# Kernel optimization log

Hardware: AMD Instinct MI355X
Metric: run time of the kernel (lower is better)

The kernel has to match this reference:

```python
import jax, jax.numpy as jnp
import numpy as np

B, N, C = 2, 2048, 2048
H, KV = 16, 4          # query heads, kv heads
D = C // H             # head_dim = 128
ROPE_BASE = 10000.0


def rope_cos_sin(position_ids, dim):
    # interleaved RoPE: freqs for even indices, repeated pairwise to full dim
    inv_freq = 1.0 / (ROPE_BASE ** (jnp.arange(0, dim, 2, dtype=jnp.float32) / dim))
    ang = position_ids[..., None].astype(jnp.float32) * inv_freq   # [B, N, D/2]
    cos = jnp.repeat(jnp.cos(ang), 2, axis=-1)                     # [B, N, D]
    sin = jnp.repeat(jnp.sin(ang), 2, axis=-1)
    return cos, sin


def rotate_half_interleaved(x):
    # (x0, x1, x2, x3, ...) -> (-x1, x0, -x3, x2, ...)
    x1 = x[..., 0::2]
    x2 = x[..., 1::2]
    return jnp.stack([-x2, x1], axis=-1).reshape(x.shape)


def apply_rotary(x, cos, sin):
    # x: [B, h, N, D]; cos/sin: [B, N, D]
    return x * cos[:, None] + rotate_half_interleaved(x) * sin[:, None]


def setup_inputs() -> dict:
    key = jax.random.key(0)
    ks = jax.random.split(key, 5)
    s = 0.02
    return dict(
        x=jax.random.normal(ks[0], (B, N, C), jnp.float32),
        position_ids=jnp.tile(jnp.arange(N, dtype=jnp.int32), (B, 1)),
        Wq=jax.random.normal(ks[1], (C, C), jnp.float32) * s,
        bq=jnp.zeros((C,), jnp.float32),
        Wk=jax.random.normal(ks[2], (C, KV * D), jnp.float32) * s,
        bk=jnp.zeros((KV * D,), jnp.float32),
        Wv=jax.random.normal(ks[3], (C, KV * D), jnp.float32) * s,
        bv=jnp.zeros((KV * D,), jnp.float32),
        Wo=jax.random.normal(ks[4], (C, C), jnp.float32) * s,
    )


def reference(x, position_ids, Wq, bq, Wk, bk, Wv, bv, Wo):
    Bx, Nx, Cx = x.shape
    q = (x @ Wq + bq).reshape(Bx, Nx, H, D).transpose(0, 2, 1, 3)   # [B,H,N,D]
    k = (x @ Wk + bk).reshape(Bx, Nx, KV, D).transpose(0, 2, 1, 3)  # [B,KV,N,D]
    v = (x @ Wv + bv).reshape(Bx, Nx, KV, D).transpose(0, 2, 1, 3)

    cos, sin = rope_cos_sin(position_ids, D)
    q = apply_rotary(q, cos, sin)
    k = apply_rotary(k, cos, sin)

    # GQA expand: head h uses kv head h // groups (matches unsqueeze+expand+reshape)
    groups = H // KV
    k = jnp.repeat(k, groups, axis=1)   # [B,H,N,D]
    v = jnp.repeat(v, groups, axis=1)

    attn = jnp.einsum('bhqd,bhkd->bhqk', q, k) * (D ** -0.5)        # [B,H,N,N]
    causal_mask = jnp.triu(jnp.ones((Nx, Nx), dtype=bool), 1)
    attn = jnp.where(causal_mask, -jnp.inf, attn)
    attn = jax.nn.softmax(attn, axis=-1)

    out = jnp.einsum('bhqk,bhkd->bhqd', attn, v)
    out = out.transpose(0, 2, 1, 3).reshape(Bx, Nx, Cx)
    return out @ Wo
```

## Files before the change

kernel.cpp:

```cpp
#include <hip/hip_runtime.h>
#include <cstdint>
#include <type_traits>

typedef unsigned short u16;
typedef unsigned int u32;
typedef __bf16 bf16x8 __attribute__((ext_vector_type(8)));
typedef float f32x4 __attribute__((ext_vector_type(4)));

constexpr int BB = 2;
constexpr int SEQ = 2048;
constexpr int CH = 2048;
constexpr int NH = 16;
constexpr int NKV = 4;
constexpr int HD = 128;
constexpr int QKVC = CH + 2 * NKV * HD;

#define DI __device__ __forceinline__

DI u16 f2b(float x) {
  u32 u = __float_as_uint(x);
  u = u + 0x7FFFu + ((u >> 16) & 1u);
  return (u16)(u >> 16);
}
DI float b2f(u16 u) { return __uint_as_float(((u32)u) << 16); }

DI u32 pack2bf(float lo, float hi) {
  return __builtin_amdgcn_perm(__float_as_uint(hi), __float_as_uint(lo), 0x07060302u);
}

DI void glds16(const void* g, void* l) {
  __builtin_amdgcn_global_load_lds(
      (__attribute__((address_space(1))) void*)(uintptr_t)g,
      (__attribute__((address_space(3))) void*)(u32)(uintptr_t)l, 16, 0, 0);
}

__global__ __launch_bounds__(256) void prep_kernel(
    const float* __restrict__ x, u16* __restrict__ xb,
    const float* __restrict__ Wq, const float* __restrict__ Wk,
    const float* __restrict__ Wv, const float* __restrict__ Wo,
    u16* __restrict__ wqkvt, u16* __restrict__ wot) {
  if (blockIdx.z == 4) {
    const int n4 = BB * SEQ * CH / 4;
    int base = (blockIdx.x + 32 * blockIdx.y) * 256 + threadIdx.x;
#pragma unroll
    for (int k = 0; k < 8; k++) {
      int i = base + k * 262144;
      if (i < n4) {
        float4 v = *(const float4*)&x[(size_t)i * 4];
        ushort4 o;
        o.x = f2b(v.x); o.y = f2b(v.y); o.z = f2b(v.z); o.w = f2b(v.w);
        *(ushort4*)&xb[(size_t)i * 4] = o;
      }
    }
    return;
  }
  const int z = blockIdx.z;
  const float* in;
  u16* out;
  int Cc;
  if (z == 0)      { in = Wq; out = wqkvt;                                Cc = CH; }
  else if (z == 1) { in = Wk; out = wqkvt + (size_t)CH * CH;              Cc = NKV * HD; }
  else if (z == 2) { in = Wv; out = wqkvt + (size_t)(CH + NKV * HD) * CH; Cc = NKV * HD; }
  else             { in = Wo; out = wot;                                  Cc = CH; }
  if ((int)blockIdx.y * 64 >= Cc) return;

  __shared__ u16 tile[64 * 65];
  const int r0 = blockIdx.x * 64, c0 = blockIdx.y * 64;
  const int tid = threadIdx.x;
  for (int c = tid; c < 1024; c += 256) {
    int r = c >> 4, col = (c & 15) * 4;
    float4 v = *(const float4*)&in[(size_t)(r0 + r) * Cc + c0 + col];
    tile[r * 65 + col + 0] = f2b(v.x);
    tile[r * 65 + col + 1] = f2b(v.y);
    tile[r * 65 + col + 2] = f2b(v.z);
    tile[r * 65 + col + 3] = f2b(v.w);
  }
  __syncthreads();
  for (int c = tid; c < 1024; c += 256) {
    int r = c >> 4, col = (c & 15) * 4;
    ushort4 v;
    v.x = tile[(col + 0) * 65 + r];
    v.y = tile[(col + 1) * 65 + r];
    v.z = tile[(col + 2) * 65 + r];
    v.w = tile[(col + 3) * 65 + r];
    *(ushort4*)&out[(size_t)(c0 + r) * CH + r0 + col] = v;
  }
}

__global__ __launch_bounds__(256) void vtrans_kernel(const u16* __restrict__ in,
                                                     u16* __restrict__ out) {
  __shared__ u16 tile[64 * 65];
  const int s = blockIdx.z, n0 = blockIdx.x * 64, d0 = blockIdx.y * 64;
  const int tid = threadIdx.x;
  const u16* ip = in + (size_t)s * SEQ * HD + (size_t)n0 * HD + d0;
  u16* op = out + (size_t)s * HD * SEQ + (size_t)d0 * SEQ + n0;
  for (int c = tid; c < 1024; c += 256) {
    int r = c >> 4, col = (c & 15) * 4;
    ushort4 v = *(const ushort4*)&ip[(size_t)r * HD + col];
    tile[r * 65 + col + 0] = v.x;
    tile[r * 65 + col + 1] = v.y;
    tile[r * 65 + col + 2] = v.z;
    tile[r * 65 + col + 3] = v.w;
  }
  __syncthreads();
  for (int c = tid; c < 1024; c += 256) {
    int r = c >> 4, col = (c & 15) * 4;
    ushort4 v;
    v.x = tile[(col + 0) * 65 + r];
    v.y = tile[(col + 1) * 65 + r];
    v.z = tile[(col + 2) * 65 + r];
    v.w = tile[(col + 3) * 65 + r];
    int u = col;
    int w = (u & 3) | (((u >> 5) & 1) << 2) | (((u >> 2) & 3) << 3) | (((u >> 4) & 1) << 5);
    int glp = (w >> 3) ^ (r & 7);
    int colp = glp * 8 + (w & 7);
    *(ushort4*)&op[(size_t)r * SEQ + colp] = v;
  }
}

template <int MODE>
__global__ __launch_bounds__(512, 2) void gemm256_kernel(
    const u16* __restrict__ A, const u16* __restrict__ Bt,
    u16* __restrict__ Qo, u16* __restrict__ Ko,
    float* __restrict__ Cf, u16* __restrict__ Vn,
    const float* __restrict__ bq, const float* __restrict__ bk,
    const float* __restrict__ bv, const int* __restrict__ pos,
    int M, int Nn, int K) {
  constexpr int BM = 128;
  constexpr int BN = (MODE == 0) ? 384 : 256;
  constexpr int NJ = (MODE == 0) ? 6 : 4;
  extern __shared__ char smem[];
  u16* As = (u16*)smem;
  u16* Bs = As + 2 * BM * 64;

  const int tid = threadIdx.x;
  const int lane = tid & 63, wave = tid >> 6;
  const int wrow = wave >> 2, wcol = wave & 3;
  const int lm = lane & 15, lq = lane >> 4;
  const int m0 = blockIdx.x * BM, n0 = blockIdx.y * BN;
  const int rr = tid >> 3;
  const int sswz8 = ((tid & 7) ^ (rr & 7)) * 8;

  f32x4 acc[4][NJ] = {};

  const int NT = K >> 6;

  if constexpr (MODE == 0) {
    auto stA = [&](int kt, int bsel, int h) {
      glds16(A + (size_t)(m0 + h * 64 + rr) * K + kt + sswz8,
             (char*)As + bsel * (BM * 128) + (h * 64 + wave * 8) * 128);
    };
    auto stB = [&](int kt, int bsel, int q, int s) {
      int g = 96 * ((s * 64 + rr) >> 5) + 32 * q + (rr & 31);
      glds16(Bt + (size_t)(n0 + g) * K + kt + sswz8,
             (char*)Bs + bsel * (BN * 128) + (q * 128 + s * 64 + wave * 8) * 128);
    };

    stA(0, 0, 0); stA(0, 0, 1);
    stB(0, 0, 0, 0); stB(0, 0, 0, 1);
    stB(0, 0, 1, 0); stB(0, 0, 1, 1);
    stB(0, 0, 2, 0); stB(0, 0, 2, 1);
    asm volatile("s_waitcnt vmcnt(0)" ::: "memory");
    __builtin_amdgcn_s_barrier();

    bf16x8 af[4][2];
    for (int T = 0; T < NT; T++) {
      const int buf = T & 1, nb = buf ^ 1;
      const u16* Asb = As + buf * (BM * 64);
      const u16* Bsb = Bs + buf * (BN * 64);
      const int kt1 = (T + 1) << 6;
      const bool pf = (T + 1 < NT);
#pragma unroll
      for (int q = 0; q < 3; q++) {
        if (q == 0) {
#pragma unroll
          for (int ii = 0; ii < 4; ii++)
#pragma unroll
            for (int kk = 0; kk < 2; kk++)
              af[ii][kk] = *(const bf16x8*)&Asb[(wrow * 64 + ii * 16 + lm) * 64 +
                                                ((kk * 4 + lq) ^ (lm & 7)) * 8];
        }
        bf16x8 bfq[2][2];
#pragma unroll
        for (int jj = 0; jj < 2; jj++)
#pragma unroll
          for (int kk = 0; kk < 2; kk++)
            bfq[jj][kk] = *(const bf16x8*)&Bsb[(q * 128 + wcol * 32 + jj * 16 + lm) * 64 +
                                               ((kk * 4 + lq) ^ (lm & 7)) * 8];
        if (pf) {
          if (q == 0) { stA(kt1, nb, 0); stA(kt1, nb, 1); stB(kt1, nb, 0, 0); stB(kt1, nb, 0, 1); }
          else if (q == 1) { stB(kt1, nb, 1, 0); stB(kt1, nb, 1, 1); }
          else { stB(kt1, nb, 2, 0); stB(kt1, nb, 2, 1); }
        }
        __builtin_amdgcn_s_barrier();
        asm volatile("s_waitcnt lgkmcnt(0)" ::: "memory");
        __builtin_amdgcn_sched_barrier(0);
        __builtin_amdgcn_s_setprio(1);
#pragma unroll
        for (int kk = 0; kk < 2; kk++)
#pragma unroll
          for (int ii = 0; ii < 4; ii++)
#pragma unroll
            for (int jj = 0; jj < 2; jj++)
              acc[ii][q * 2 + jj] = __builtin_amdgcn_mfma_f32_16x16x32_bf16(
                  af[ii][kk], bfq[jj][kk], acc[ii][q * 2 + jj], 0, 0, 0);
        __builtin_amdgcn_s_setprio(0);
        if (q == 0) {
          if (pf) asm volatile("s_waitcnt vmcnt(6)" ::: "memory");
          else    asm volatile("s_waitcnt vmcnt(2)" ::: "memory");
        } else if (q == 1) {
          if (pf) asm volatile("s_waitcnt vmcnt(6)" ::: "memory");
          else    asm volatile("s_waitcnt vmcnt(0)" ::: "memory");
        } else if (pf) {
          asm volatile("s_waitcnt vmcnt(4)" ::: "memory");
        }
        __builtin_amdgcn_s_barrier();
      }
    }
  } else {
    auto stageA = [&](int kt, int bsel, int half) {
      const int rb = (wave & 3) * 8 + (wave >> 2) * 64 + half * 32;
      glds16(A + (size_t)(m0 + rb + (lane >> 3)) * K + kt + sswz8,
             (char*)As + bsel * (BM * 128) + rb * 128);
    };
    auto stageB = [&](int kt, int bsel, int half) {
#pragma unroll
      for (int j = 0; j < 2; j++) {
        const int rb = (wave & 3) * 8 + (j * 2 + (wave >> 2)) * 64 + half * 32;
        glds16(Bt + (size_t)(n0 + rb + (lane >> 3)) * K + kt + sswz8,
               (char*)Bs + bsel * 32768 + rb * 128);
      }
    };

    stageA(0, 0, 0); stageB(0, 0, 0); stageB(0, 0, 1); stageA(0, 0, 1);
    asm volatile("s_waitcnt vmcnt(0)" ::: "memory");
    __builtin_amdgcn_s_barrier();

    bf16x8 bf1[4][2];
    for (int T = 0; T < NT; T++) {
      const int buf = T & 1;
      const u16* Asb = As + buf * (BM * 64);
      const u16* Bsb = Bs + buf * (256 * 64);
      const int kt1 = (T + 1) << 6;
      const bool pf = (T + 1 < NT);
      bf16x8 af[2][2];
#pragma unroll
      for (int q = 0; q < 2; q++) {
#pragma unroll
        for (int ii = 0; ii < 2; ii++)
#pragma unroll
          for (int kk = 0; kk < 2; kk++)
            af[ii][kk] = *(const bf16x8*)&Asb[(wrow * 64 + (q * 2 + ii) * 16 + lm) * 64 +
                                              ((kk * 4 + lq) ^ (lm & 7)) * 8];
        if (q == 0) {
#pragma unroll
          for (int j = 0; j < 4; j++)
#pragma unroll
            for (int kk = 0; kk < 2; kk++)
              bf1[j][kk] = *(const bf16x8*)&Bsb[(wcol * 64 + j * 16 + lm) * 64 +
                                                ((kk * 4 + lq) ^ (lm & 7)) * 8];
        }
        if (pf) {
          if (q == 0) { stageA(kt1, buf ^ 1, 0); stageB(kt1, buf ^ 1, 0); stageB(kt1, buf ^ 1, 1); }
          else stageA(kt1, buf ^ 1, 1);
        }
        __builtin_amdgcn_s_barrier();
        asm volatile("s_waitcnt lgkmcnt(0)" ::: "memory");
        __builtin_amdgcn_sched_barrier(0);
        __builtin_amdgcn_s_setprio(1);
#pragma unroll
        for (int kk = 0; kk < 2; kk++)
#pragma unroll
          for (int ii = 0; ii < 2; ii++)
#pragma unroll
            for (int j = 0; j < 4; j++)
              acc[q * 2 + ii][j] = __builtin_amdgcn_mfma_f32_16x16x32_bf16(
                  af[ii][kk], bf1[j][kk], acc[q * 2 + ii][j], 0, 0, 0);
        __builtin_amdgcn_s_setprio(0);
        if (q == 0) {
          if (pf) asm volatile("s_waitcnt vmcnt(5)" ::: "memory");
          else    asm volatile("s_waitcnt vmcnt(0)" ::: "memory");
        } else if (pf) {
          asm volatile("s_waitcnt vmcnt(1)" ::: "memory");
        }
        __builtin_amdgcn_s_barrier();
      }
    }
  }

  if constexpr (MODE == 0) {
    __syncthreads();
    float2* tab = (float2*)smem;
    const float LN1E4_64 = 0.14391156831212788f;
    for (int e = tid; e < 128 * 64; e += 512) {
      int tk = e >> 6, ii = e & 63;
      float ang = (float)pos[m0 + tk] * expf(-(float)ii * LN1E4_64);
      float sn, cs;
      sincosf(ang, &sn, &cs);
      tab[e] = make_float2(cs, sn);
    }
    __syncthreads();
    const float SCL2G = 0.12754325f;

#pragma unroll
    for (int i = 0; i < 4; i++) {
      const int mg = m0 + wrow * 64 + i * 16 + lq * 4;
#pragma unroll
      for (int j = 0; j < NJ; j++) {
        const int ng = n0 + wcol * 96 + j * 16 + lm;
        const int reg7 = (n0 + wcol * 96 + j * 16) >> 7;
        float bias = (ng < CH) ? bq[ng]
                               : (ng < CH + NKV * HD ? bk[ng - CH] : bv[ng - CH - NKV * HD]);
        if (reg7 < 16) {
          const int d = ng & 127, ii = d >> 1, hh = ng >> 7;
#pragma unroll
          for (int r = 0; r < 4; r++) {
            float v = acc[i][j][r] + bias;
            float vp = __shfl_xor(v, 1);
            float2 cw = tab[(mg + r - m0) * 64 + ii];
            float c = cw.x * SCL2G, s = cw.y * SCL2G;
            float o = fmaf(v, c, (lane & 1) ? vp * s : -(vp * s));
            int tok = mg + r, bb2 = tok >> 11, n = tok & (SEQ - 1);
            Qo[((size_t)(bb2 * NH + hh) * SEQ + n) * HD + d] = f2b(o);
          }
        } else if (reg7 < 20) {
          const int d = ng & 127, ii = d >> 1, kh = (ng >> 7) - 16, g = d >> 3;
#pragma unroll
          for (int r = 0; r < 4; r++) {
            float v = acc[i][j][r] + bias;
            float vp = __shfl_xor(v, 1);
            float2 cw = tab[(mg + r - m0) * 64 + ii];
            float o = fmaf(v, cw.x, (lane & 1) ? vp * cw.y : -(vp * cw.y));
            int tok = mg + r, bb2 = tok >> 11, n = tok & (SEQ - 1);
            int gp = (g & 8) | ((g ^ n) & 7);
            Ko[((size_t)(bb2 * NKV + kh) * SEQ + n) * HD + gp * 8 + (d & 7)] = f2b(o);
          }
        } else {
          const int vcol = ng - (CH + NKV * HD), kh = vcol >> 7, d = vcol & (HD - 1);
#pragma unroll
          for (int r = 0; r < 4; r++) {
            float v = acc[i][j][r] + bias;
            int tok = mg + r, bb2 = tok >> 11, n = tok & (SEQ - 1);
            Vn[((size_t)(bb2 * NKV + kh) * SEQ + n) * HD + d] = f2b(v);
          }
        }
      }
    }
  } else {
#pragma unroll
    for (int i = 0; i < 4; i++) {
      const int mg = m0 + wrow * 64 + i * 16 + lq * 4;
#pragma unroll
      for (int j = 0; j < NJ; j++) {
        const int ng = n0 + wcol * (NJ * 16) + j * 16 + lm;
#pragma unroll
        for (int r = 0; r < 4; r++)
          Cf[(size_t)(mg + r) * Nn + ng] = acc[i][j][r];
      }
    }
  }
}

__global__ __launch_bounds__(256, 2) void flash_kernel(
    const u16* __restrict__ Q, const u16* __restrict__ Kk,
    const u16* __restrict__ Vt, u16* __restrict__ Oo) {
  __shared__ u16 Kb[2][64 * 128];
  __shared__ u16 Vb[2][144 * 64];
  const int tid = threadIdx.x, lane = tid & 63, wave = tid >> 6;
  const int lm = lane & 15, lq = lane >> 4;
  const int p = blockIdx.x;
  const int h = blockIdx.y, b = blockIdx.z;
  const int q0A = p * 64, q0B = (31 - p) * 64;
  const int kvh = h >> 2;
  const u16* Qg = Q + (size_t)(b * NH + h) * SEQ * HD;
  const u16* Kg = Kk + (size_t)(b * NKV + kvh) * SEQ * HD;
  const u16* Vg = Vt + (size_t)(b * NKV + kvh) * HD * SEQ;

  if (tid < 128) Vb[tid >> 6][128 * 64 + (tid & 63)] = 0x3F80;

  bf16x8 qf[2][4];
#pragma unroll
  for (int qg = 0; qg < 2; qg++) {
    const int q0g = qg ? q0B : q0A;
    const u16* qrow = Qg + (size_t)(q0g + wave * 16 + lm) * HD;
#pragma unroll
    for (int kd = 0; kd < 4; kd++)
      qf[qg][kd] = *(const bf16x8*)&qrow[kd * 32 + lq * 8];
  }

  f32x4 oacc[2][8] = {};
  f32x4 oaccS[2] = {};
  const int nIter = 32 - p;

  auto stage = [&](int kv0, int bufi) {
    const char* kb = (const char*)(Kg + (size_t)kv0 * HD);
    char* kl = (char*)&Kb[bufi][0];
    const char* vbb = (const char*)(Vg + (size_t)kv0);
    char* vl = (char*)&Vb[bufi][0];
#pragma unroll
    for (int c = 0; c < 4; c++) {
      int ch = wave * 4 + c;
      glds16(kb + ch * 1024 + lane * 16, kl + ch * 1024);
      glds16(vbb + (size_t)(ch * 8 + (lane >> 3)) * (SEQ * 2) + (lane & 7) * 16,
             vl + ch * 1024);
    }
  };

  stage(0, 0);

  for (int t = 0; t < nIter; t++) {
    __syncthreads();
    if (t + 1 < nIter) stage((t + 1) * 64, (t + 1) & 1);
    const u16* Ks = &Kb[t & 1][0];
    const u16* Vs = &Vb[t & 1][0];
    const int kv0 = t * 64;
    const bool actA = (t <= p);

    auto run = [&](auto dualc) {
      constexpr bool DUAL = decltype(dualc)::value;
      f32x4 sv[2][4] = {};
#pragma unroll
      for (int nt = 0; nt < 4; nt++)
#pragma unroll
        for (int kd = 0; kd < 4; kd++) {
          int g = kd * 4 + lq;
          int gpp = (g & 8) | ((g ^ lm) & 7);
          bf16x8 kf = *(const bf16x8*)&Ks[(nt * 16 + lm) * 128 + gpp * 8];
          sv[1][nt] = __builtin_amdgcn_mfma_f32_16x16x32_bf16(kf, qf[1][kd], sv[1][nt], 0, 0, 0);
          if constexpr (DUAL)
            sv[0][nt] = __builtin_amdgcn_mfma_f32_16x16x32_bf16(kf, qf[0][kd], sv[0][nt], 0, 0, 0);
        }

      alignas(16) u32 pad[2][2][4];
      auto softmax = [&](int qg, int q0g) {
        const int base = q0g + wave * 16;
        if (kv0 + 63 > base) {
          const int qrow = base + lm;
#pragma unroll
          for (int nt = 0; nt < 4; nt++) {
            float pv[4];
#pragma unroll
            for (int r = 0; r < 4; r++) {
              int kvg = kv0 + nt * 16 + lq * 4 + r;
              float e = exp2f(sv[qg][nt][r]);
              pv[r] = (kvg > qrow) ? 0.f : e;
            }
            pad[qg][nt & 1][(nt >> 1) * 2 + 0] = pack2bf(pv[0], pv[1]);
            pad[qg][nt & 1][(nt >> 1) * 2 + 1] = pack2bf(pv[2], pv[3]);
          }
        } else {
#pragma unroll
          for (int nt = 0; nt < 4; nt++) {
            float pv[4];
#pragma unroll
            for (int r = 0; r < 4; r++) pv[r] = exp2f(sv[qg][nt][r]);
            pad[qg][nt & 1][(nt >> 1) * 2 + 0] = pack2bf(pv[0], pv[1]);
            pad[qg][nt & 1][(nt >> 1) * 2 + 1] = pack2bf(pv[2], pv[3]);
          }
        }
      };
      softmax(1, q0B);
      if constexpr (DUAL) softmax(0, q0A);

#pragma unroll
      for (int ks = 0; ks < 2; ks++) {
        const int glp = (ks * 4 + lq) ^ (lm & 7);
        const bf16x8 pa1 = *(const bf16x8*)&pad[1][ks][0];
        const bf16x8 pa0 = *(const bf16x8*)&pad[0][ks][0];
#pragma unroll
        for (int dt = 0; dt < 8; dt++) {
          bf16x8 vf = *(const bf16x8*)&Vs[(dt * 16 + lm) * 64 + glp * 8];
          oacc[1][dt] = __builtin_amdgcn_mfma_f32_16x16x32_bf16(pa1, vf, oacc[1][dt], 0, 0, 0);
          if constexpr (DUAL)
            oacc[0][dt] = __builtin_amdgcn_mfma_f32_16x16x32_bf16(pa0, vf, oacc[0][dt], 0, 0, 0);
        }
        bf16x8 vf8 = *(const bf16x8*)&Vs[(128 + lm) * 64 + glp * 8];
        oaccS[1] = __builtin_amdgcn_mfma_f32_16x16x32_bf16(pa1, vf8, oaccS[1], 0, 0, 0);
        if constexpr (DUAL)
          oaccS[0] = __builtin_amdgcn_mfma_f32_16x16x32_bf16(pa0, vf8, oaccS[0], 0, 0, 0);
      }
    };
    if (actA) run(std::integral_constant<bool, true>{});
    else      run(std::integral_constant<bool, false>{});
  }

  u16* orow = Oo + (size_t)b * SEQ * CH + (size_t)h * HD;
#pragma unroll
  for (int qg = 0; qg < 2; qg++) {
    const int q0g = qg ? q0B : q0A;
    float inv[4];
#pragma unroll
    for (int r = 0; r < 4; r++) inv[r] = 1.0f / __shfl(oaccS[qg][r], lq * 16);
    const int qrow_base = q0g + wave * 16 + lq * 4;
#pragma unroll
    for (int dt = 0; dt < 8; dt++)
#pragma unroll
      for (int r = 0; r < 4; r++)
        orow[(size_t)(qrow_base + r) * CH + dt * 16 + lm] = f2b(oacc[qg][dt][r] * inv[r]);
  }
}

extern "C" void kernel_launch(void* const* d_in, const int* in_sizes, int n_in,
                              void* d_out, int out_size, void* d_ws, size_t ws_size,
                              hipStream_t stream) {
  const float* x = (const float*)d_in[0];
  const int* pos = (const int*)d_in[1];
  const float* Wq = (const float*)d_in[2];
  const float* bq = (const float*)d_in[3];
  const float* Wk = (const float*)d_in[4];
  const float* bk = (const float*)d_in[5];
  const float* Wv = (const float*)d_in[6];
  const float* bv = (const float*)d_in[7];
  const float* Wo = (const float*)d_in[8];
  float* out = (float*)d_out;

  char* ws = (char*)d_ws;
  u16* xb = (u16*)ws;    ws += (size_t)BB * SEQ * CH * 2;
  u16* wqkvt = (u16*)ws; ws += (size_t)QKVC * CH * 2;
  u16* wot = (u16*)ws;   ws += (size_t)CH * CH * 2;
  u16* qr = (u16*)ws;    ws += (size_t)BB * NH * SEQ * HD * 2;
  u16* kr = (u16*)ws;    ws += (size_t)BB * NKV * SEQ * HD * 2;
  u16* vn = (u16*)ws;    ws += (size_t)BB * NKV * SEQ * HD * 2;
  u16* vt = (u16*)ws;    ws += (size_t)BB * NKV * SEQ * HD * 2;
  u16* ao = (u16*)ws;    ws += (size_t)BB * SEQ * CH * 2;

  static int attr_done = 0;
  if (!attr_done) {
    hipFuncSetAttribute(reinterpret_cast<const void*>(gemm256_kernel<0>),
                        hipFuncAttributeMaxDynamicSharedMemorySize, 131072);
    hipFuncSetAttribute(reinterpret_cast<const void*>(gemm256_kernel<1>),
                        hipFuncAttributeMaxDynamicSharedMemorySize, 131072);
    attr_done = 1;
  }

  prep_kernel<<<dim3(32, 32, 5), 256, 0, stream>>>(x, xb, Wq, Wk, Wv, Wo, wqkvt, wot);
  gemm256_kernel<0><<<dim3(32, 8), 512, 131072, stream>>>(
      xb, wqkvt, qr, kr, (float*)nullptr, vn, bq, bk, bv, pos, BB * SEQ, QKVC, CH);
  vtrans_kernel<<<dim3(SEQ / 64, HD / 64, BB * NKV), 256, 0, stream>>>(vn, vt);
  flash_kernel<<<dim3(16, NH, BB), 256, 0, stream>>>(qr, kr, vt, ao);
  gemm256_kernel<1><<<dim3(32, 8), 512, 98304, stream>>>(
      ao, wot, nullptr, nullptr, out, nullptr, nullptr, nullptr, nullptr, nullptr,
      BB * SEQ, CH, CH);
}
```

Baseline: 287.2 us.

## Shrink GEMM tiles to 4-wave blocks with single-buffered A staging

Both projection GEMMs move from 512-thread blocks with 128x384/128x256 tiles to 256-thread blocks with 128x192/128x128 tiles, doubling grid size to 512 blocks. The LDS pipeline is reorganized: the QKV GEMM drops double buffering entirely and interleaves next-tile loads within the q-phases, while the output GEMM double-buffers only B with A single-buffered. This reduces LDS per block and should improve occupancy and wave-level load balance across CUs. The tradeoff is lower per-block data reuse and tighter load/compute overlap that may expose memory latency.

```diff
diff --git a/kernel.cpp b/kernel.cpp
--- a/kernel.cpp
+++ b/kernel.cpp
@@ -119,7 +119,7 @@
 }
 
 template <int MODE>
-__global__ __launch_bounds__(512, 2) void gemm256_kernel(
+__global__ __launch_bounds__(256, 2) void gemm4w_kernel(
     const u16* __restrict__ A, const u16* __restrict__ Bt,
     u16* __restrict__ Qo, u16* __restrict__ Ko,
     float* __restrict__ Cf, u16* __restrict__ Vn,
@@ -127,48 +127,44 @@
     const float* __restrict__ bv, const int* __restrict__ pos,
     int M, int Nn, int K) {
   constexpr int BM = 128;
-  constexpr int BN = (MODE == 0) ? 384 : 256;
+  constexpr int BN = (MODE == 0) ? 192 : 128;
   constexpr int NJ = (MODE == 0) ? 6 : 4;
   extern __shared__ char smem[];
   u16* As = (u16*)smem;
-  u16* Bs = As + 2 * BM * 64;
+  u16* Bs = As + 128 * 64;
 
   const int tid = threadIdx.x;
   const int lane = tid & 63, wave = tid >> 6;
-  const int wrow = wave >> 2, wcol = wave & 3;
+  const int wrow = wave >> 1, wcol = wave & 1;
   const int lm = lane & 15, lq = lane >> 4;
   const int m0 = blockIdx.x * BM, n0 = blockIdx.y * BN;
   const int rr = tid >> 3;
   const int sswz8 = ((tid & 7) ^ (rr & 7)) * 8;
 
   f32x4 acc[4][NJ] = {};
-
   const int NT = K >> 6;
 
+  auto stA = [&](int kt, int s) {
+    glds16(A + (size_t)(m0 + 32 * s + rr) * K + kt + sswz8,
+           (char*)As + (32 * s + wave * 8) * 128);
+  };
+  auto stB = [&](int kt, int s, int bsel) {
+    int g0 = (MODE == 0) ? (96 * (s & 1) + 32 * (s >> 1))
+                         : (64 * (s & 1) + 32 * (s >> 1));
+    glds16(Bt + (size_t)(n0 + g0 + rr) * K + kt + sswz8,
+           (char*)Bs + bsel * 16384 + (32 * s + wave * 8) * 128);
+  };
+
   if constexpr (MODE == 0) {
-    auto stA = [&](int kt, int bsel, int h) {
-      glds16(A + (size_t)(m0 + h * 64 + rr) * K + kt + sswz8,
-             (char*)As + bsel * (BM * 128) + (h * 64 + wave * 8) * 128);
-    };
-    auto stB = [&](int kt, int bsel, int q, int s) {
-      int g = 96 * ((s * 64 + rr) >> 5) + 32 * q + (rr & 31);
-      glds16(Bt + (size_t)(n0 + g) * K + kt + sswz8,
-             (char*)Bs + bsel * (BN * 128) + (q * 128 + s * 64 + wave * 8) * 128);
-    };
-
-    stA(0, 0, 0); stA(0, 0, 1);
-    stB(0, 0, 0, 0); stB(0, 0, 0, 1);
-    stB(0, 0, 1, 0); stB(0, 0, 1, 1);
-    stB(0, 0, 2, 0); stB(0, 0, 2, 1);
-    asm volatile("s_waitcnt vmcnt(0)" ::: "memory");
+    stA(0, 0); stA(0, 1); stA(0, 2); stA(0, 3);
+    stB(0, 0, 0); stB(0, 1, 0);
+    stB(0, 2, 0); stB(0, 3, 0);
+    asm volatile("s_waitcnt vmcnt(2)" ::: "memory");
     __builtin_amdgcn_s_barrier();
 
     bf16x8 af[4][2];
     for (int T = 0; T < NT; T++) {
-      const int buf = T & 1, nb = buf ^ 1;
-      const u16* Asb = As + buf * (BM * 64);
-      const u16* Bsb = Bs + buf * (BN * 64);
-      const int kt1 = (T + 1) << 6;
+      const int kt = T << 6, kt1 = (T + 1) << 6;
       const bool pf = (T + 1 < NT);
 #pragma unroll
       for (int q = 0; q < 3; q++) {
@@ -177,21 +173,20 @@
           for (int ii = 0; ii < 4; ii++)
 #pragma unroll
             for (int kk = 0; kk < 2; kk++)
-              af[ii][kk] = *(const bf16x8*)&Asb[(wrow * 64 + ii * 16 + lm) * 64 +
-                                                ((kk * 4 + lq) ^ (lm & 7)) * 8];
+              af[ii][kk] = *(const bf16x8*)&As[(wrow * 64 + ii * 16 + lm) * 64 +
+                                               ((kk * 4 + lq) ^ (lm & 7)) * 8];
         }
         bf16x8 bfq[2][2];
 #pragma unroll
         for (int jj = 0; jj < 2; jj++)
 #pragma unroll
           for (int kk = 0; kk < 2; kk++)
-            bfq[jj][kk] = *(const bf16x8*)&Bsb[(q * 128 + wcol * 32 + jj * 16 + lm) * 64 +
-                                               ((kk * 4 + lq) ^ (lm & 7)) * 8];
-        if (pf) {
-          if (q == 0) { stA(kt1, nb, 0); stA(kt1, nb, 1); stB(kt1, nb, 0, 0); stB(kt1, nb, 0, 1); }
-          else if (q == 1) { stB(kt1, nb, 1, 0); stB(kt1, nb, 1, 1); }
-          else { stB(kt1, nb, 2, 0); stB(kt1, nb, 2, 1); }
-        }
+            bfq[jj][kk] = *(const bf16x8*)&Bs[(64 * q + wcol * 32 + jj * 16 + lm) * 64 +
+                                              ((kk * 4 + lq) ^ (lm & 7)) * 8];
+        if (q == 0) { stB(kt, 4, 0); stB(kt, 5, 0); }
+        else if (q == 1 && pf) { stA(kt1, 0); stA(kt1, 1); stA(kt1, 2); stA(kt1, 3);
+                                 stB(kt1, 0, 0); stB(kt1, 1, 0); }
+        else if (q == 2 && pf) { stB(kt1, 2, 0); stB(kt1, 3, 0); }
         __builtin_amdgcn_s_barrier();
         asm volatile("s_waitcnt lgkmcnt(0)" ::: "memory");
         __builtin_amdgcn_sched_barrier(0);
@@ -206,63 +201,51 @@
                   af[ii][kk], bfq[jj][kk], acc[ii][q * 2 + jj], 0, 0, 0);
         __builtin_amdgcn_s_setprio(0);
         if (q == 0) {
-          if (pf) asm volatile("s_waitcnt vmcnt(6)" ::: "memory");
-          else    asm volatile("s_waitcnt vmcnt(2)" ::: "memory");
+          asm volatile("s_waitcnt vmcnt(2)" ::: "memory");
         } else if (q == 1) {
           if (pf) asm volatile("s_waitcnt vmcnt(6)" ::: "memory");
           else    asm volatile("s_waitcnt vmcnt(0)" ::: "memory");
         } else if (pf) {
-          asm volatile("s_waitcnt vmcnt(4)" ::: "memory");
+          asm volatile("s_waitcnt vmcnt(2)" ::: "memory");
         }
         __builtin_amdgcn_s_barrier();
       }
     }
   } else {
-    auto stageA = [&](int kt, int bsel, int half) {
-      const int rb = (wave & 3) * 8 + (wave >> 2) * 64 + half * 32;
-      glds16(A + (size_t)(m0 + rb + (lane >> 3)) * K + kt + sswz8,
-             (char*)As + bsel * (BM * 128) + rb * 128);
-    };
-    auto stageB = [&](int kt, int bsel, int half) {
-#pragma unroll
-      for (int j = 0; j < 2; j++) {
-        const int rb = (wave & 3) * 8 + (j * 2 + (wave >> 2)) * 64 + half * 32;
-        glds16(Bt + (size_t)(n0 + rb + (lane >> 3)) * K + kt + sswz8,
-               (char*)Bs + bsel * 32768 + rb * 128);
-      }
-    };
-
-    stageA(0, 0, 0); stageB(0, 0, 0); stageB(0, 0, 1); stageA(0, 0, 1);
-    asm volatile("s_waitcnt vmcnt(0)" ::: "memory");
+    stB(0, 0, 0); stB(0, 1, 0);
+    stA(0, 0); stA(0, 1); stA(0, 2); stA(0, 3);
+    stB(0, 2, 0); stB(0, 3, 0);
+    asm volatile("s_waitcnt vmcnt(2)" ::: "memory");
     __builtin_amdgcn_s_barrier();
 
-    bf16x8 bf1[4][2];
+    bf16x8 af[4][2];
     for (int T = 0; T < NT; T++) {
-      const int buf = T & 1;
-      const u16* Asb = As + buf * (BM * 64);
-      const u16* Bsb = Bs + buf * (256 * 64);
+      const int bsel = T & 1, nbs = bsel ^ 1;
       const int kt1 = (T + 1) << 6;
       const bool pf = (T + 1 < NT);
-      bf16x8 af[2][2];
 #pragma unroll
       for (int q = 0; q < 2; q++) {
-#pragma unroll
-        for (int ii = 0; ii < 2; ii++)
+        if (q == 0) {
+#pragma unroll
+          for (int ii = 0; ii < 4; ii++)
+#pragma unroll
+            for (int kk = 0; kk < 2; kk++)
+              af[ii][kk] = *(const bf16x8*)&As[(wrow * 64 + ii * 16 + lm) * 64 +
+                                               ((kk * 4 + lq) ^ (lm & 7)) * 8];
+        }
+        bf16x8 bfq[2][2];
+#pragma unroll
+        for (int jj = 0; jj < 2; jj++)
 #pragma unroll
           for (int kk = 0; kk < 2; kk++)
-            af[ii][kk] = *(const bf16x8*)&Asb[(wrow * 64 + (q * 2 + ii) * 16 + lm) * 64 +
+            bfq[jj][kk] = *(const bf16x8*)&Bs[bsel * 8192 +
+                                              (64 * q + wcol * 32 + jj * 16 + lm) * 64 +
                                               ((kk * 4 + lq) ^ (lm & 7)) * 8];
         if (q == 0) {
-#pragma unroll
-          for (int j = 0; j < 4; j++)
-#pragma unroll
-            for (int kk = 0; kk < 2; kk++)
-              bf1[j][kk] = *(const bf16x8*)&Bsb[(wcol * 64 + j * 16 + lm) * 64 +
-                                                ((kk * 4 + lq) ^ (lm & 7)) * 8];
-        }
-        if (pf) {
-          if (q == 0) { stageA(kt1, buf ^ 1, 0); stageB(kt1, buf ^ 1, 0); stageB(kt1, buf ^ 1, 1); }
-          else stageA(kt1, buf ^ 1, 1);
+          if (pf) { stB(kt1, 0, nbs); stB(kt1, 1, nbs); }
+        } else if (pf) {
+          stA(kt1, 0); stA(kt1, 1); stA(kt1, 2); stA(kt1, 3);
+          stB(kt1, 2, nbs); stB(kt1, 3, nbs);
         }
         __builtin_amdgcn_s_barrier();
         asm volatile("s_waitcnt lgkmcnt(0)" ::: "memory");
@@ -271,17 +254,17 @@
 #pragma unroll
         for (int kk = 0; kk < 2; kk++)
 #pragma unroll
-          for (int ii = 0; ii < 2; ii++)
-#pragma unroll
-            for (int j = 0; j < 4; j++)
-              acc[q * 2 + ii][j] = __builtin_amdgcn_mfma_f32_16x16x32_bf16(
-                  af[ii][kk], bf1[j][kk], acc[q * 2 + ii][j], 0, 0, 0);
+          for (int ii = 0; ii < 4; ii++)
+#pragma unroll
+            for (int jj = 0; jj < 2; jj++)
+              acc[ii][q * 2 + jj] = __builtin_amdgcn_mfma_f32_16x16x32_bf16(
+                  af[ii][kk], bfq[jj][kk], acc[ii][q * 2 + jj], 0, 0, 0);
         __builtin_amdgcn_s_setprio(0);
         if (q == 0) {
-          if (pf) asm volatile("s_waitcnt vmcnt(5)" ::: "memory");
+          if (pf) asm volatile("s_waitcnt vmcnt(2)" ::: "memory");
           else    asm volatile("s_waitcnt vmcnt(0)" ::: "memory");
         } else if (pf) {
-          asm volatile("s_waitcnt vmcnt(1)" ::: "memory");
+          asm volatile("s_waitcnt vmcnt(2)" ::: "memory");
         }
         __builtin_amdgcn_s_barrier();
       }
@@ -292,7 +275,7 @@
     __syncthreads();
     float2* tab = (float2*)smem;
     const float LN1E4_64 = 0.14391156831212788f;
-    for (int e = tid; e < 128 * 64; e += 512) {
+    for (int e = tid; e < 128 * 64; e += 256) {
       int tk = e >> 6, ii = e & 63;
       float ang = (float)pos[m0 + tk] * expf(-(float)ii * LN1E4_64);
       float sn, cs;
@@ -352,7 +335,7 @@
       const int mg = m0 + wrow * 64 + i * 16 + lq * 4;
 #pragma unroll
       for (int j = 0; j < NJ; j++) {
-        const int ng = n0 + wcol * (NJ * 16) + j * 16 + lm;
+        const int ng = n0 + wcol * 64 + j * 16 + lm;
 #pragma unroll
         for (int r = 0; r < 4; r++)
           Cf[(size_t)(mg + r) * Nn + ng] = acc[i][j][r];
@@ -526,19 +509,19 @@
 
   static int attr_done = 0;
   if (!attr_done) {
-    hipFuncSetAttribute(reinterpret_cast<const void*>(gemm256_kernel<0>),
+    hipFuncSetAttribute(reinterpret_cast<const void*>(gemm4w_kernel<0>),
                         hipFuncAttributeMaxDynamicSharedMemorySize, 131072);
-    hipFuncSetAttribute(reinterpret_cast<const void*>(gemm256_kernel<1>),
+    hipFuncSetAttribute(reinterpret_cast<const void*>(gemm4w_kernel<1>),
                         hipFuncAttributeMaxDynamicSharedMemorySize, 131072);
     attr_done = 1;
   }
 
   prep_kernel<<<dim3(32, 32, 5), 256, 0, stream>>>(x, xb, Wq, Wk, Wv, Wo, wqkvt, wot);
-  gemm256_kernel<0><<<dim3(32, 8), 512, 131072, stream>>>(
+  gemm4w_kernel<0><<<dim3(32, 16), 256, 65536, stream>>>(
       xb, wqkvt, qr, kr, (float*)nullptr, vn, bq, bk, bv, pos, BB * SEQ, QKVC, CH);
   vtrans_kernel<<<dim3(SEQ / 64, HD / 64, BB * NKV), 256, 0, stream>>>(vn, vt);
   flash_kernel<<<dim3(16, NH, BB), 256, 0, stream>>>(qr, kr, vt, ao);
-  gemm256_kernel<1><<<dim3(32, 8), 512, 98304, stream>>>(
+  gemm4w_kernel<1><<<dim3(32, 16), 256, 49152, stream>>>(
       ao, wot, nullptr, nullptr, out, nullptr, nullptr, nullptr, nullptr, nullptr,
       BB * SEQ, CH, CH);
 }
```

Result: no change. 288.5 us (+0.4%).

## Fuse V transpose into QKV GEMM epilogue and retile GEMM to 128x192

Applied to the files above, without the earlier changes.

The separate vtrans kernel is removed: the QKV GEMM epilogue now writes V directly in the transposed, swizzled layout the flash kernel expects, using 4-element vector stores along the sequence. The QKV GEMM is also retiled to 256-thread blocks of 128x192 on a 32x16 grid, with a single-buffered shared-memory scheme that interleaves the next tile's loads with compute. This removes one launch and a full V round-trip through memory, and doubles the block count. The cost is less double-buffering slack and extra barrier exposure in the reshaped pipeline.

```diff
diff --git a/kernel.cpp b/kernel.cpp
--- a/kernel.cpp
+++ b/kernel.cpp
@@ -87,48 +87,163 @@
   }
 }
 
-__global__ __launch_bounds__(256) void vtrans_kernel(const u16* __restrict__ in,
-                                                     u16* __restrict__ out) {
-  __shared__ u16 tile[64 * 65];
-  const int s = blockIdx.z, n0 = blockIdx.x * 64, d0 = blockIdx.y * 64;
-  const int tid = threadIdx.x;
-  const u16* ip = in + (size_t)s * SEQ * HD + (size_t)n0 * HD + d0;
-  u16* op = out + (size_t)s * HD * SEQ + (size_t)d0 * SEQ + n0;
-  for (int c = tid; c < 1024; c += 256) {
-    int r = c >> 4, col = (c & 15) * 4;
-    ushort4 v = *(const ushort4*)&ip[(size_t)r * HD + col];
-    tile[r * 65 + col + 0] = v.x;
-    tile[r * 65 + col + 1] = v.y;
-    tile[r * 65 + col + 2] = v.z;
-    tile[r * 65 + col + 3] = v.w;
-  }
-  __syncthreads();
-  for (int c = tid; c < 1024; c += 256) {
-    int r = c >> 4, col = (c & 15) * 4;
-    ushort4 v;
-    v.x = tile[(col + 0) * 65 + r];
-    v.y = tile[(col + 1) * 65 + r];
-    v.z = tile[(col + 2) * 65 + r];
-    v.w = tile[(col + 3) * 65 + r];
-    int u = col;
-    int w = (u & 3) | (((u >> 5) & 1) << 2) | (((u >> 2) & 3) << 3) | (((u >> 4) & 1) << 5);
-    int glp = (w >> 3) ^ (r & 7);
-    int colp = glp * 8 + (w & 7);
-    *(ushort4*)&op[(size_t)r * SEQ + colp] = v;
-  }
-}
-
-template <int MODE>
-__global__ __launch_bounds__(512, 2) void gemm256_kernel(
+__global__ __launch_bounds__(256, 2) void gemm0_kernel(
     const u16* __restrict__ A, const u16* __restrict__ Bt,
-    u16* __restrict__ Qo, u16* __restrict__ Ko,
-    float* __restrict__ Cf, u16* __restrict__ Vn,
+    u16* __restrict__ Qo, u16* __restrict__ Ko, u16* __restrict__ Vt,
     const float* __restrict__ bq, const float* __restrict__ bk,
     const float* __restrict__ bv, const int* __restrict__ pos,
     int M, int Nn, int K) {
   constexpr int BM = 128;
-  constexpr int BN = (MODE == 0) ? 384 : 256;
-  constexpr int NJ = (MODE == 0) ? 6 : 4;
+  constexpr int NJ = 6;
+  extern __shared__ char smem[];
+  u16* As = (u16*)smem;
+  u16* Bs = As + 128 * 64;
+
+  const int tid = threadIdx.x;
+  const int lane = tid & 63, wave = tid >> 6;
+  const int wrow = wave >> 1, wcol = wave & 1;
+  const int lm = lane & 15, lq = lane >> 4;
+  const int m0 = blockIdx.x * BM, n0 = blockIdx.y * 192;
+  const int rr = tid >> 3;
+  const int sswz8 = ((tid & 7) ^ (rr & 7)) * 8;
+
+  f32x4 acc[4][NJ] = {};
+  const int NT = K >> 6;
+
+  auto stA = [&](int kt, int s) {
+    glds16(A + (size_t)(m0 + 32 * s + rr) * K + kt + sswz8,
+           (char*)As + (32 * s + wave * 8) * 128);
+  };
+  auto stB = [&](int kt, int s) {
+    int g0 = 96 * (s & 1) + 32 * (s >> 1);
+    glds16(Bt + (size_t)(n0 + g0 + rr) * K + kt + sswz8,
+           (char*)Bs + (32 * s + wave * 8) * 128);
+  };
+
+  stA(0, 0); stA(0, 1); stA(0, 2); stA(0, 3);
+  stB(0, 0); stB(0, 1);
+  stB(0, 2); stB(0, 3);
+  asm volatile("s_waitcnt vmcnt(2)" ::: "memory");
+  __builtin_amdgcn_s_barrier();
+
+  bf16x8 af[4][2];
+  for (int T = 0; T < NT; T++) {
+    const int kt = T << 6, kt1 = (T + 1) << 6;
+    const bool pf = (T + 1 < NT);
+#pragma unroll
+    for (int q = 0; q < 3; q++) {
+      if (q == 0) {
+#pragma unroll
+        for (int ii = 0; ii < 4; ii++)
+#pragma unroll
+          for (int kk = 0; kk < 2; kk++)
+            af[ii][kk] = *(const bf16x8*)&As[(wrow * 64 + ii * 16 + lm) * 64 +
+                                             ((kk * 4 + lq) ^ (lm & 7)) * 8];
+      }
+      bf16x8 bfq[2][2];
+#pragma unroll
+      for (int jj = 0; jj < 2; jj++)
+#pragma unroll
+        for (int kk = 0; kk < 2; kk++)
+          bfq[jj][kk] = *(const bf16x8*)&Bs[(64 * q + wcol * 32 + jj * 16 + lm) * 64 +
+                                            ((kk * 4 + lq) ^ (lm & 7)) * 8];
+      if (q == 0) { stB(kt, 4); stB(kt, 5); }
+      else if (q == 1 && pf) { stA(kt1, 0); stA(kt1, 1); stA(kt1, 2); stA(kt1, 3);
+                               stB(kt1, 0); stB(kt1, 1); }
+      else if (q == 2 && pf) { stB(kt1, 2); stB(kt1, 3); }
+      __builtin_amdgcn_s_barrier();
+      asm volatile("s_waitcnt lgkmcnt(0)" ::: "memory");
+      __builtin_amdgcn_sched_barrier(0);
+      __builtin_amdgcn_s_setprio(1);
+#pragma unroll
+      for (int kk = 0; kk < 2; kk++)
+#pragma unroll
+        for (int ii = 0; ii < 4; ii++)
+#pragma unroll
+          for (int jj = 0; jj < 2; jj++)
+            acc[ii][q * 2 + jj] = __builtin_amdgcn_mfma_f32_16x16x32_bf16(
+                af[ii][kk], bfq[jj][kk], acc[ii][q * 2 + jj], 0, 0, 0);
+      __builtin_amdgcn_s_setprio(0);
+      if (q == 0) {
+        asm volatile("s_waitcnt vmcnt(2)" ::: "memory");
+      } else if (q == 1) {
+        if (pf) asm volatile("s_waitcnt vmcnt(6)" ::: "memory");
+        else    asm volatile("s_waitcnt vmcnt(0)" ::: "memory");
+      } else if (pf) {
+        asm volatile("s_waitcnt vmcnt(2)" ::: "memory");
+      }
+      __builtin_amdgcn_s_barrier();
+    }
+  }
+
+  __syncthreads();
+  float2* tab = (float2*)smem;
+  const float LN1E4_64 = 0.14391156831212788f;
+  for (int e = tid; e < 128 * 64; e += 256) {
+    int tk = e >> 6, ii = e & 63;
+    float ang = (float)pos[m0 + tk] * expf(-(float)ii * LN1E4_64);
+    float sn, cs;
+    sincosf(ang, &sn, &cs);
+    tab[e] = make_float2(cs, sn);
+  }
+  __syncthreads();
+  const float SCL2G = 0.12754325f;
+
+#pragma unroll
+  for (int i = 0; i < 4; i++) {
+    const int mg = m0 + wrow * 64 + i * 16 + lq * 4;
+#pragma unroll
+    for (int j = 0; j < NJ; j++) {
+      const int ng = n0 + wcol * 96 + j * 16 + lm;
+      const int reg7 = (n0 + wcol * 96 + j * 16) >> 7;
+      float bias = (ng < CH) ? bq[ng]
+                             : (ng < CH + NKV * HD ? bk[ng - CH] : bv[ng - CH - NKV * HD]);
+      if (reg7 < 16) {
+        const int d = ng & 127, ii = d >> 1, hh = ng >> 7;
+#pragma unroll
+        for (int r = 0; r < 4; r++) {
+          float v = acc[i][j][r] + bias;
+          float vp = __shfl_xor(v, 1);
+          float2 cw = tab[(mg + r - m0) * 64 + ii];
+          float c = cw.x * SCL2G, s = cw.y * SCL2G;
+          float o = fmaf(v, c, (lane & 1) ? vp * s : -(vp * s));
+          int tok = mg + r, bb2 = tok >> 11, n = tok & (SEQ - 1);
+          Qo[((size_t)(bb2 * NH + hh) * SEQ + n) * HD + d] = f2b(o);
+        }
+      } else if (reg7 < 20) {
+        const int d = ng & 127, ii = d >> 1, kh = (ng >> 7) - 16, g = d >> 3;
+#pragma unroll
+        for (int r = 0; r < 4; r++) {
+          float v = acc[i][j][r] + bias;
+          float vp = __shfl_xor(v, 1);
+          float2 cw = tab[(mg + r - m0) * 64 + ii];
+          float o = fmaf(v, cw.x, (lane & 1) ? vp * cw.y : -(vp * cw.y));
+          int tok = mg + r, bb2 = tok >> 11, n = tok & (SEQ - 1);
+          int gp = (g & 8) | ((g ^ n) & 7);
+          Ko[((size_t)(bb2 * NKV + kh) * SEQ + n) * HD + gp * 8 + (d & 7)] = f2b(o);
+        }
+      } else {
+        const int vcol = ng - (CH + NKV * HD), kh = vcol >> 7, d = vcol & (HD - 1);
+        const int tok0 = mg, bb2 = tok0 >> 11, n0t = tok0 & (SEQ - 1);
+        const int u = n0t & 63;
+        const int w = (u & 3) | (((u >> 5) & 1) << 2) | (((u >> 2) & 3) << 3) |
+                      (((u >> 4) & 1) << 5);
+        const int colp = ((((w >> 3) ^ (d & 7)) << 3) | (w & 7));
+        ushort4 vv;
+        vv.x = f2b(acc[i][j][0] + bias);
+        vv.y = f2b(acc[i][j][1] + bias);
+        vv.z = f2b(acc[i][j][2] + bias);
+        vv.w = f2b(acc[i][j][3] + bias);
+        *(ushort4*)&Vt[((size_t)(bb2 * NKV + kh) * HD + d) * SEQ + (n0t & ~63) + colp] = vv;
+      }
+    }
+  }
+}
+
+__global__ __launch_bounds__(512, 2) void gemm1_kernel(
+    const u16* __restrict__ A, const u16* __restrict__ Bt,
+    float* __restrict__ Cf, int M, int Nn, int K) {
+  constexpr int BM = 128;
   extern __shared__ char smem[];
   u16* As = (u16*)smem;
   u16* Bs = As + 2 * BM * 64;
@@ -137,226 +252,91 @@
   const int lane = tid & 63, wave = tid >> 6;
   const int wrow = wave >> 2, wcol = wave & 3;
   const int lm = lane & 15, lq = lane >> 4;
-  const int m0 = blockIdx.x * BM, n0 = blockIdx.y * BN;
+  const int m0 = blockIdx.x * BM, n0 = blockIdx.y * 256;
   const int rr = tid >> 3;
   const int sswz8 = ((tid & 7) ^ (rr & 7)) * 8;
 
-  f32x4 acc[4][NJ] = {};
-
+  f32x4 acc[4][4] = {};
   const int NT = K >> 6;
 
-  if constexpr (MODE == 0) {
-    auto stA = [&](int kt, int bsel, int h) {
-      glds16(A + (size_t)(m0 + h * 64 + rr) * K + kt + sswz8,
-             (char*)As + bsel * (BM * 128) + (h * 64 + wave * 8) * 128);
-    };
-    auto stB = [&](int kt, int bsel, int q, int s) {
-      int g = 96 * ((s * 64 + rr) >> 5) + 32 * q + (rr & 31);
-      glds16(Bt + (size_t)(n0 + g) * K + kt + sswz8,
-             (char*)Bs + bsel * (BN * 128) + (q * 128 + s * 64 + wave * 8) * 128);
-    };
-
-    stA(0, 0, 0); stA(0, 0, 1);
-    stB(0, 0, 0, 0); stB(0, 0, 0, 1);
-    stB(0, 0, 1, 0); stB(0, 0, 1, 1);
-    stB(0, 0, 2, 0); stB(0, 0, 2, 1);
-    asm volatile("s_waitcnt vmcnt(0)" ::: "memory");
-    __builtin_amdgcn_s_barrier();
-
-    bf16x8 af[4][2];
-    for (int T = 0; T < NT; T++) {
-      const int buf = T & 1, nb = buf ^ 1;
-      const u16* Asb = As + buf * (BM * 64);
-      const u16* Bsb = Bs + buf * (BN * 64);
-      const int kt1 = (T + 1) << 6;
-      const bool pf = (T + 1 < NT);
-#pragma unroll
-      for (int q = 0; q < 3; q++) {
-        if (q == 0) {
-#pragma unroll
-          for (int ii = 0; ii < 4; ii++)
-#pragma unroll
-            for (int kk = 0; kk < 2; kk++)
-              af[ii][kk] = *(const bf16x8*)&Asb[(wrow * 64 + ii * 16 + lm) * 64 +
-                                                ((kk * 4 + lq) ^ (lm & 7)) * 8];
-        }
-        bf16x8 bfq[2][2];
-#pragma unroll
-        for (int jj = 0; jj < 2; jj++)
+  auto stageA = [&](int kt, int bsel, int half) {
+    const int rb = (wave & 3) * 8 + (wave >> 2) * 64 + half * 32;
+    glds16(A + (size_t)(m0 + rb + (lane >> 3)) * K + kt + sswz8,
+           (char*)As + bsel * (BM * 128) + rb * 128);
+  };
+  auto stageB = [&](int kt, int bsel, int half) {
+#pragma unroll
+    for (int j = 0; j < 2; j++) {
+      const int rb = (wave & 3) * 8 + (j * 2 + (wave >> 2)) * 64 + half * 32;
+      glds16(Bt + (size_t)(n0 + rb + (lane >> 3)) * K + kt + sswz8,
+             (char*)Bs + bsel * 32768 + rb * 128);
+    }
+  };
+
+  stageA(0, 0, 0); stageB(0, 0, 0); stageB(0, 0, 1); stageA(0, 0, 1);
+  asm volatile("s_waitcnt vmcnt(0)" ::: "memory");
+  __builtin_amdgcn_s_barrier();
+
+  bf16x8 bf1[4][2];
+  for (int T = 0; T < NT; T++) {
+    const int buf = T & 1;
+    const u16* Asb = As + buf * (BM * 64);
+    const u16* Bsb = Bs + buf * (256 * 64);
+    const int kt1 = (T + 1) << 6;
+    const bool pf = (T + 1 < NT);
+    bf16x8 af[2][2];
+#pragma unroll
+    for (int q = 0; q < 2; q++) {
+#pragma unroll
+      for (int ii = 0; ii < 2; ii++)
+#pragma unroll
+        for (int kk = 0; kk < 2; kk++)
+          af[ii][kk] = *(const bf16x8*)&Asb[(wrow * 64 + (q * 2 + ii) * 16 + lm) * 64 +
+                                            ((kk * 4 + lq) ^ (lm & 7)) * 8];
+      if (q == 0) {
+#pragma unroll
+        for (int j = 0; j < 4; j++)
 #pragma unroll
           for (int kk = 0; kk < 2; kk++)
-            bfq[jj][kk] = *(const bf16x8*)&Bsb[(q * 128 + wcol * 32 + jj * 16 + lm) * 64 +
-                                               ((kk * 4 + lq) ^ (lm & 7)) * 8];
-        if (pf) {
-          if (q == 0) { stA(kt1, nb, 0); stA(kt1, nb, 1); stB(kt1, nb, 0, 0); stB(kt1, nb, 0, 1); }
-          else if (q == 1) { stB(kt1, nb, 1, 0); stB(kt1, nb, 1, 1); }
-          else { stB(kt1, nb, 2, 0); stB(kt1, nb, 2, 1); }
-        }
-        __builtin_amdgcn_s_barrier();
-        asm volatile("s_waitcnt lgkmcnt(0)" ::: "memory");
-        __builtin_amdgcn_sched_barrier(0);
-        __builtin_amdgcn_s_setprio(1);
-#pragma unroll
-        for (int kk = 0; kk < 2; kk++)
-#pragma unroll
-          for (int ii = 0; ii < 4; ii++)
-#pragma unroll
-            for (int jj = 0; jj < 2; jj++)
-              acc[ii][q * 2 + jj] = __builtin_amdgcn_mfma_f32_16x16x32_bf16(
-                  af[ii][kk], bfq[jj][kk], acc[ii][q * 2 + jj], 0, 0, 0);
-        __builtin_amdgcn_s_setprio(0);
-        if (q == 0) {
-          if (pf) asm volatile("s_waitcnt vmcnt(6)" ::: "memory");
-          else    asm volatile("s_waitcnt vmcnt(2)" ::: "memory");
-        } else if (q == 1) {
-          if (pf) asm volatile("s_waitcnt vmcnt(6)" ::: "memory");
-          else    asm volatile("s_waitcnt vmcnt(0)" ::: "memory");
-        } else if (pf) {
-          asm volatile("s_waitcnt vmcnt(4)" ::: "memory");
-        }
-        __builtin_amdgcn_s_barrier();
-      }
-    }
-  } else {
-    auto stageA = [&](int kt, int bsel, int half) {
-      const int rb = (wave & 3) * 8 + (wave >> 2) * 64 + half * 32;
-      glds16(A + (size_t)(m0 + rb + (lane >> 3)) * K + kt + sswz8,
-             (char*)As + bsel * (BM * 128) + rb * 128);
-    };
-    auto stageB = [&](int kt, int bsel, int half) {
-#pragma unroll
-      for (int j = 0; j < 2; j++) {
-        const int rb = (wave & 3) * 8 + (j * 2 + (wave >> 2)) * 64 + half * 32;
-        glds16(Bt + (size_t)(n0 + rb + (lane >> 3)) * K + kt + sswz8,
-               (char*)Bs + bsel * 32768 + rb * 128);
-      }
-    };
-
-    stageA(0, 0, 0); stageB(0, 0, 0); stageB(0, 0, 1); stageA(0, 0, 1);
-    asm volatile("s_waitcnt vmcnt(0)" ::: "memory");
-    __builtin_amdgcn_s_barrier();
-
-    bf16x8 bf1[4][2];
-    for (int T = 0; T < NT; T++) {
-      const int buf = T & 1;
-      const u16* Asb = As + buf * (BM * 64);
-      const u16* Bsb = Bs + buf * (256 * 64);
-      const int kt1 = (T + 1) << 6;
-      const bool pf = (T + 1 < NT);
-      bf16x8 af[2][2];
-#pragma unroll
-      for (int q = 0; q < 2; q++) {
+            bf1[j][kk] = *(const bf16x8*)&Bsb[(wcol * 64 + j * 16 + lm) * 64 +
+                                              ((kk * 4 + lq) ^ (lm & 7)) * 8];
+      }
+      if (pf) {
+        if (q == 0) { stageA(kt1, buf ^ 1, 0); stageB(kt1, buf ^ 1, 0); stageB(kt1, buf ^ 1, 1); }
+        else stageA(kt1, buf ^ 1, 1);
+      }
+      __builtin_amdgcn_s_barrier();
+      asm volatile("s_waitcnt lgkmcnt(0)" ::: "memory");
+      __builtin_amdgcn_sched_barrier(0);
+      __builtin_amdgcn_s_setprio(1);
+#pragma unroll
+      for (int kk = 0; kk < 2; kk++)
 #pragma unroll
         for (int ii = 0; ii < 2; ii++)
 #pragma unroll
-          for (int kk = 0; kk < 2; kk++)
-            af[ii][kk] = *(const bf16x8*)&Asb[(wrow * 64 + (q * 2 + ii) * 16 + lm) * 64 +
-                                              ((kk * 4 + lq) ^ (lm & 7)) * 8];
-        if (q == 0) {
-#pragma unroll
           for (int j = 0; j < 4; j++)
-#pragma unroll
-            for (int kk = 0; kk < 2; kk++)
-              bf1[j][kk] = *(const bf16x8*)&Bsb[(wcol * 64 + j * 16 + lm) * 64 +
-                                                ((kk * 4 + lq) ^ (lm & 7)) * 8];
-        }
-        if (pf) {
-          if (q == 0) { stageA(kt1, buf ^ 1, 0); stageB(kt1, buf ^ 1, 0); stageB(kt1, buf ^ 1, 1); }
-          else stageA(kt1, buf ^ 1, 1);
-        }
-        __builtin_amdgcn_s_barrier();
-        asm volatile("s_waitcnt lgkmcnt(0)" ::: "memory");
-        __builtin_amdgcn_sched_barrier(0);
-        __builtin_amdgcn_s_setprio(1);
-#pragma unroll
-        for (int kk = 0; kk < 2; kk++)
-#pragma unroll
-          for (int ii = 0; ii < 2; ii++)
-#pragma unroll
-            for (int j = 0; j < 4; j++)
-              acc[q * 2 + ii][j] = __builtin_amdgcn_mfma_f32_16x16x32_bf16(
-                  af[ii][kk], bf1[j][kk], acc[q * 2 + ii][j], 0, 0, 0);
-        __builtin_amdgcn_s_setprio(0);
-        if (q == 0) {
-          if (pf) asm volatile("s_waitcnt vmcnt(5)" ::: "memory");
-          else    asm volatile("s_waitcnt vmcnt(0)" ::: "memory");
-        } else if (pf) {
-          asm volatile("s_waitcnt vmcnt(1)" ::: "memory");
-        }
-        __builtin_amdgcn_s_barrier();
-      }
-    }
-  }
-
-  if constexpr (MODE == 0) {
-    __syncthreads();
-    float2* tab = (float2*)smem;
-    const float LN1E4_64 = 0.14391156831212788f;
-    for (int e = tid; e < 128 * 64; e += 512) {
-      int tk = e >> 6, ii = e & 63;
-      float ang = (float)pos[m0 + tk] * expf(-(float)ii * LN1E4_64);
-      float sn, cs;
-      sincosf(ang, &sn, &cs);
-      tab[e] = make_float2(cs, sn);
-    }
-    __syncthreads();
-    const float SCL2G = 0.12754325f;
-
-#pragma unroll
-    for (int i = 0; i < 4; i++) {
-      const int mg = m0 + wrow * 64 + i * 16 + lq * 4;
-#pragma unroll
-      for (int j = 0; j < NJ; j++) {
-        const int ng = n0 + wcol * 96 + j * 16 + lm;
-        const int reg7 = (n0 + wcol * 96 + j * 16) >> 7;
-        float bias = (ng < CH) ? bq[ng]
-                               : (ng < CH + NKV * HD ? bk[ng - CH] : bv[ng - CH - NKV * HD]);
-        if (reg7 < 16) {
-          const int d = ng & 127, ii = d >> 1, hh = ng >> 7;
-#pragma unroll
-          for (int r = 0; r < 4; r++) {
-            float v = acc[i][j][r] + bias;
-            float vp = __shfl_xor(v, 1);
-            float2 cw = tab[(mg + r - m0) * 64 + ii];
-            float c = cw.x * SCL2G, s = cw.y * SCL2G;
-            float o = fmaf(v, c, (lane & 1) ? vp * s : -(vp * s));
-            int tok = mg + r, bb2 = tok >> 11, n = tok & (SEQ - 1);
-            Qo[((size_t)(bb2 * NH + hh) * SEQ + n) * HD + d] = f2b(o);
-          }
-        } else if (reg7 < 20) {
-          const int d = ng & 127, ii = d >> 1, kh = (ng >> 7) - 16, g = d >> 3;
-#pragma unroll
-          for (int r = 0; r < 4; r++) {
-            float v = acc[i][j][r] + bias;
-            float vp = __shfl_xor(v, 1);
-            float2 cw = tab[(mg + r - m0) * 64 + ii];
-            float o = fmaf(v, cw.x, (lane & 1) ? vp * cw.y : -(vp * cw.y));
-            int tok = mg + r, bb2 = tok >> 11, n = tok & (SEQ - 1);
-            int gp = (g & 8) | ((g ^ n) & 7);
-            Ko[((size_t)(bb2 * NKV + kh) * SEQ + n) * HD + gp * 8 + (d & 7)] = f2b(o);
-          }
-        } else {
-          const int vcol = ng - (CH + NKV * HD), kh = vcol >> 7, d = vcol & (HD - 1);
-#pragma unroll
-          for (int r = 0; r < 4; r++) {
-            float v = acc[i][j][r] + bias;
-            int tok = mg + r, bb2 = tok >> 11, n = tok & (SEQ - 1);
-            Vn[((size_t)(bb2 * NKV + kh) * SEQ + n) * HD + d] = f2b(v);
-          }
-        }
-      }
-    }
-  } else {
-#pragma unroll
-    for (int i = 0; i < 4; i++) {
-      const int mg = m0 + wrow * 64 + i * 16 + lq * 4;
-#pragma unroll
-      for (int j = 0; j < NJ; j++) {
-        const int ng = n0 + wcol * (NJ * 16) + j * 16 + lm;
-#pragma unroll
-        for (int r = 0; r < 4; r++)
-          Cf[(size_t)(mg + r) * Nn + ng] = acc[i][j][r];
-      }
+            acc[q * 2 + ii][j] = __builtin_amdgcn_mfma_f32_16x16x32_bf16(
+                af[ii][kk], bf1[j][kk], acc[q * 2 + ii][j], 0, 0, 0);
+      __builtin_amdgcn_s_setprio(0);
+      if (q == 0) {
+        if (pf) asm volatile("s_waitcnt vmcnt(5)" ::: "memory");
+        else    asm volatile("s_waitcnt vmcnt(0)" ::: "memory");
+      } else if (pf) {
+        asm volatile("s_waitcnt vmcnt(1)" ::: "memory");
+      }
+      __builtin_amdgcn_s_barrier();
+    }
+  }
+
+#pragma unroll
+  for (int i = 0; i < 4; i++) {
+    const int mg = m0 + wrow * 64 + i * 16 + lq * 4;
+#pragma unroll
+    for (int j = 0; j < 4; j++) {
+      const int ng = n0 + wcol * 64 + j * 16 + lm;
+#pragma unroll
+      for (int r = 0; r < 4; r++)
+        Cf[(size_t)(mg + r) * Nn + ng] = acc[i][j][r];
     }
   }
 }
@@ -520,25 +500,21 @@
   u16* wot = (u16*)ws;   ws += (size_t)CH * CH * 2;
   u16* qr = (u16*)ws;    ws += (size_t)BB * NH * SEQ * HD * 2;
   u16* kr = (u16*)ws;    ws += (size_t)BB * NKV * SEQ * HD * 2;
-  u16* vn = (u16*)ws;    ws += (size_t)BB * NKV * SEQ * HD * 2;
   u16* vt = (u16*)ws;    ws += (size_t)BB * NKV * SEQ * HD * 2;
   u16* ao = (u16*)ws;    ws += (size_t)BB * SEQ * CH * 2;
 
   static int attr_done = 0;
   if (!attr_done) {
-    hipFuncSetAttribute(reinterpret_cast<const void*>(gemm256_kernel<0>),
+    hipFuncSetAttribute(reinterpret_cast<const void*>(gemm0_kernel),
                         hipFuncAttributeMaxDynamicSharedMemorySize, 131072);
-    hipFuncSetAttribute(reinterpret_cast<const void*>(gemm256_kernel<1>),
+    hipFuncSetAttribute(reinterpret_cast<const void*>(gemm1_kernel),
                         hipFuncAttributeMaxDynamicSharedMemorySize, 131072);
     attr_done = 1;
   }
 
   prep_kernel<<<dim3(32, 32, 5), 256, 0, stream>>>(x, xb, Wq, Wk, Wv, Wo, wqkvt, wot);
-  gemm256_kernel<0><<<dim3(32, 8), 512, 131072, stream>>>(
-      xb, wqkvt, qr, kr, (float*)nullptr, vn, bq, bk, bv, pos, BB * SEQ, QKVC, CH);
-  vtrans_kernel<<<dim3(SEQ / 64, HD / 64, BB * NKV), 256, 0, stream>>>(vn, vt);
+  gemm0_kernel<<<dim3(32, 16), 256, 65536, stream>>>(
+      xb, wqkvt, qr, kr, vt, bq, bk, bv, pos, BB * SEQ, QKVC, CH);
   flash_kernel<<<dim3(16, NH, BB), 256, 0, stream>>>(qr, kr, vt, ao);
-  gemm256_kernel<1><<<dim3(32, 8), 512, 98304, stream>>>(
-      ao, wot, nullptr, nullptr, out, nullptr, nullptr, nullptr, nullptr, nullptr,
-      BB * SEQ, CH, CH);
-}
+  gemm1_kernel<<<dim3(32, 8), 512, 98304, stream>>>(ao, wot, out, BB * SEQ, CH, CH);
+}
```

Result: slower. 294.1 us (+2.4%).
